# Kernel optimization log

Hardware: AMD Instinct MI355X
Metric: run time of the kernel (lower is better)

Reference implementation:

```python
import jax, jax.numpy as jnp
import numpy as np

N_HEAD = 16
D_K = 64
D_V = 64
D_MODEL = 1024
EPS = 1e-6
NEG = -1e9


def layer_norm(x, gamma, beta):
    mu = jnp.mean(x, axis=-1, keepdims=True)
    var = jnp.var(x, axis=-1, keepdims=True)
    return (x - mu) * jax.lax.rsqrt(var + EPS) * gamma + beta


def setup_inputs() -> dict:
    key = jax.random.key(0)
    ks = jax.random.split(key, 8)
    B, L = 2, 2048
    q = jax.random.normal(ks[0], (B, L, D_MODEL), dtype=jnp.float32)
    k = jax.random.normal(ks[1], (B, L, D_MODEL), dtype=jnp.float32)
    v = jax.random.normal(ks[2], (B, L, D_MODEL), dtype=jnp.float32)
    mask = jnp.ones((L, L), dtype=jnp.int32)
    s = 1.0 / np.sqrt(D_MODEL)
    w_q = jax.random.normal(ks[3], (N_HEAD * D_K, D_MODEL), dtype=jnp.float32) * s
    w_k = jax.random.normal(ks[4], (N_HEAD * D_K, D_MODEL), dtype=jnp.float32) * s
    w_v = jax.random.normal(ks[5], (N_HEAD * D_V, D_MODEL), dtype=jnp.float32) * s
    w_o = jax.random.normal(ks[6], (D_MODEL, N_HEAD * D_V), dtype=jnp.float32) * s
    ln_g = jnp.ones((D_MODEL,), dtype=jnp.float32)
    ln_b = jnp.zeros((D_MODEL,), dtype=jnp.float32)
    return {"q": q, "k": k, "v": v, "mask": mask,
            "w_q": w_q, "w_k": w_k, "w_v": w_v, "w_o": w_o,
            "ln_g": ln_g, "ln_b": ln_b}


def reference(q, k, v, mask, w_q, w_k, w_v, w_o, ln_g, ln_b):
    B, Lq, _ = q.shape
    Lk = k.shape[1]
    residual = q
    qn = layer_norm(q, ln_g, ln_b)
    # projections (nn.Linear: x @ W^T), reshape to [B, H, L, d]
    Q = (qn @ w_q.T).reshape(B, Lq, N_HEAD, D_K).transpose(0, 2, 1, 3)
    K = (k @ w_k.T).reshape(B, Lk, N_HEAD, D_K).transpose(0, 2, 1, 3)
    V = (v @ w_v.T).reshape(B, Lk, N_HEAD, D_V).transpose(0, 2, 1, 3)
    temp = jnp.asarray(D_K ** 0.5, dtype=Q.dtype)
    attn = jnp.einsum('bhqd,bhkd->bhqk', Q / temp, K)
    attn = jnp.where(mask[None, None] == 0, jnp.asarray(NEG, attn.dtype), attn)
    attn = jax.nn.softmax(attn, axis=-1)  # dropout is identity in eval
    out = jnp.einsum('bhqk,bhkd->bhqd', attn, V)
    out = out.transpose(0, 2, 1, 3).reshape(B, Lq, N_HEAD * D_V)
    out = out @ w_o.T
    return out + residual
```

## Files before the change

kernel.cpp:

```cpp
#include <hip/hip_runtime.h>
#include <stdint.h>

typedef __attribute__((ext_vector_type(8))) short bf16x8;
typedef __attribute__((ext_vector_type(4))) short s16x4;
typedef __attribute__((ext_vector_type(4))) float f32x4;

__device__ __forceinline__ ushort f2bf(float f) {
  union { float f; uint32_t u; } c; c.f = f;
  uint32_t r = (c.u + 0x7fffu + ((c.u >> 16) & 1u)) >> 16;
  return (ushort)r;
}

__device__ __forceinline__ void gload16(const void* g, void* l) {
  __builtin_amdgcn_global_load_lds(
      (const __attribute__((address_space(1))) void*)g,
      (__attribute__((address_space(3))) void*)l, 16, 0, 0);
}

__device__ __forceinline__ unsigned lds_addr(const void* p) {
  return (unsigned)(uintptr_t)(__attribute__((address_space(3))) const char*)p;
}

__device__ __forceinline__ uint32_t cvtpk(float lo, float hi) {
  uint32_t d;
  asm("v_cvt_pk_bf16_f32 %0, %1, %2" : "=v"(d) : "v"(lo), "v"(hi));
  return d;
}

__global__ __launch_bounds__(256) void prep_kernel(
    const float* __restrict__ q, const float* __restrict__ k,
    const float* __restrict__ v, const float* __restrict__ w_q,
    const float* __restrict__ w_k, const float* __restrict__ w_v,
    const float* __restrict__ w_o, const float* __restrict__ ln_g,
    const float* __restrict__ ln_b,
    ushort* __restrict__ qn, ushort* __restrict__ kb, ushort* __restrict__ vb,
    ushort* __restrict__ wqb, ushort* __restrict__ wkb,
    ushort* __restrict__ wvb, ushort* __restrict__ wob) {
  const int bid = blockIdx.x;
  const int t = threadIdx.x;
  if (bid < 4096) {
    const int row = bid;
    const float4 val = ((const float4*)(q + (size_t)row * 1024))[t];
    float s  = val.x + val.y + val.z + val.w;
    float s2 = val.x*val.x + val.y*val.y + val.z*val.z + val.w*val.w;
    #pragma unroll
    for (int off = 1; off < 64; off <<= 1) {
      s  += __shfl_xor(s,  off);
      s2 += __shfl_xor(s2, off);
    }
    __shared__ float red[8];
    const int wave = t >> 6, lane = t & 63;
    if (lane == 0) { red[wave*2] = s; red[wave*2+1] = s2; }
    __syncthreads();
    s  = red[0] + red[2] + red[4] + red[6];
    s2 = red[1] + red[3] + red[5] + red[7];
    const float mu = s * (1.0f/1024.0f);
    const float var = s2 * (1.0f/1024.0f) - mu*mu;
    const float rs = rsqrtf(var + 1e-6f);
    const float4 gg = ((const float4*)ln_g)[t];
    const float4 bb = ((const float4*)ln_b)[t];
    ushort4 o;
    o.x = f2bf((val.x - mu) * rs * gg.x + bb.x);
    o.y = f2bf((val.y - mu) * rs * gg.y + bb.y);
    o.z = f2bf((val.z - mu) * rs * gg.z + bb.z);
    o.w = f2bf((val.w - mu) * rs * gg.w + bb.w);
    ((ushort4*)(qn + (size_t)row * 1024))[t] = o;
    return;
  }
  const float* in; ushort* out; int i;
  if (bid < 12288) {
    const int idx = bid - 4096;
    const bool isv = idx >= 4096;
    in  = isv ? v : k;
    out = isv ? vb : kb;
    i = (idx & 4095) * 256 + t;
  } else {
    const int idx = bid - 12288;
    const int w = idx >> 10;
    in  = w == 0 ? w_q : (w == 1 ? w_k : (w == 2 ? w_v : w_o));
    out = w == 0 ? wqb : (w == 1 ? wkb : (w == 2 ? wvb : wob));
    i = (idx & 1023) * 256 + t;
  }
  const float4 val = ((const float4*)in)[i];
  ushort4 o;
  o.x = f2bf(val.x); o.y = f2bf(val.y); o.z = f2bf(val.z); o.w = f2bf(val.w);
  ((ushort4*)out)[i] = o;
}

__global__ __launch_bounds__(256) void mask_flags(
    const int* __restrict__ mask, int* __restrict__ flags) {
  const int qt = blockIdx.y, kt = blockIdx.x;
  const int t = threadIdx.x;
  const int* p = mask + (size_t)(qt * 64 + (t >> 2)) * 2048 + kt * 64 + (t & 3) * 16;
  int ok = 1;
  #pragma unroll
  for (int i = 0; i < 4; i++) {
    const int4 m = ((const int4*)p)[i];
    ok &= (m.x != 0) & (m.y != 0) & (m.z != 0) & (m.w != 0);
  }
  __shared__ int sok;
  if (t == 0) sok = 1;
  __syncthreads();
  if (!ok) atomicAnd(&sok, 0);
  __syncthreads();
  if (t == 0) flags[qt * 32 + kt] = sok;
}

__global__ __launch_bounds__(256, 3) void gemm3(
    const ushort* __restrict__ A0, const ushort* __restrict__ W0, ushort* __restrict__ C0,
    const ushort* __restrict__ A1, const ushort* __restrict__ W1, ushort* __restrict__ C1,
    const ushort* __restrict__ A2, const ushort* __restrict__ W2, ushort* __restrict__ C2,
    float qscale) {
  __shared__ ushort As[3][4096];
  __shared__ ushort Bs[3][4096];
  const int t = threadIdx.x, lane = t & 63, wave = t >> 6;
  const int wr = wave >> 1, wc = wave & 1;
  const int lr = lane & 15, lg = lane >> 4;
  const int lin = blockIdx.x;
  const int swz = (lin & 7) * 96 + (lin >> 3);
  const int brow = ((swz >> 3) & 31) * 128, bcol = (swz & 7) * 128;
  const int z = swz >> 8;
  const ushort* A = z == 0 ? A0 : (z == 1 ? A1 : A2);
  const ushort* W = z == 0 ? W0 : (z == 1 ? W1 : W2);
  ushort*      C = z == 0 ? C0 : (z == 1 ? C1 : C2);
  const float sc = (z == 0) ? qscale : 1.0f;
  f32x4 acc[4][4] = {};
  const int r_ = t >> 2, cx = (t & 3) ^ ((r_ >> 1) & 3);
  const ushort* gA  = A + (size_t)(brow + r_) * 1024 + cx * 8;
  const ushort* gB  = W + (size_t)(bcol + r_) * 1024 + cx * 8;
  const ushort* gA2 = gA + 64 * 1024;
  const ushort* gB2 = gB + 64 * 1024;
  const int woff = wave * 1024;
  char* const la0 = (char*)As[0] + woff;
  char* const la1 = (char*)As[1] + woff;
  char* const la2 = (char*)As[2] + woff;
  char* const lb0 = (char*)Bs[0] + woff;
  char* const lb1 = (char*)Bs[1] + woff;
  char* const lb2 = (char*)Bs[2] + woff;
  const int xA = ((lr >> 1) & 3) * 8;

#define G_ISSUE_U(LA, LB, OFF) { \
    gload16(gA  + (OFF), (LA));        gload16(gA2 + (OFF), (LA) + 4096); \
    gload16(gB  + (OFF), (LB));        gload16(gB2 + (OFF), (LB) + 4096); }

#define G_COMPUTE_U(BI) { \
    const ushort* as_ = As[BI]; \
    const ushort* bs_ = Bs[BI]; \
    bf16x8 af[4], bfr[4]; \
    _Pragma("unroll") for (int i = 0; i < 4; i++) \
      af[i]  = *(const bf16x8*)&as_[(wr*64 + i*16 + lr) * 32 + ((lg*8) ^ xA)]; \
    _Pragma("unroll") for (int i = 0; i < 4; i++) \
      bfr[i] = *(const bf16x8*)&bs_[(wc*64 + i*16 + lr) * 32 + ((lg*8) ^ xA)]; \
    _Pragma("unroll") for (int mi = 0; mi < 4; mi++) \
      _Pragma("unroll") for (int ni = 0; ni < 4; ni++) \
        acc[mi][ni] = __builtin_amdgcn_mfma_f32_16x16x32_bf16(af[mi], bfr[ni], acc[mi][ni], 0, 0, 0); }

  G_ISSUE_U(la0, lb0, 0);
  G_ISSUE_U(la1, lb1, 32);
  for (int k = 0; k < 10; ++k) {
    asm volatile("s_waitcnt vmcnt(4)" ::: "memory");
    __builtin_amdgcn_s_barrier();
    G_ISSUE_U(la2, lb2, 64);
    G_COMPUTE_U(0);
    asm volatile("s_waitcnt vmcnt(4)" ::: "memory");
    __builtin_amdgcn_s_barrier();
    G_ISSUE_U(la0, lb0, 96);
    G_COMPUTE_U(1);
    asm volatile("s_waitcnt vmcnt(4)" ::: "memory");
    __builtin_amdgcn_s_barrier();
    G_ISSUE_U(la1, lb1, 128);
    G_COMPUTE_U(2);
    gA += 96; gA2 += 96; gB += 96; gB2 += 96;
  }
  asm volatile("s_waitcnt vmcnt(4)" ::: "memory");
  __builtin_amdgcn_s_barrier();
  G_COMPUTE_U(0);
  asm volatile("s_waitcnt vmcnt(0)" ::: "memory");
  __builtin_amdgcn_s_barrier();
  G_COMPUTE_U(1);
#undef G_ISSUE_U
#undef G_COMPUTE_U

  #pragma unroll
  for (int mi = 0; mi < 4; mi++) {
    #pragma unroll
    for (int ni = 0; ni < 4; ni++) {
      #pragma unroll
      for (int r = 0; r < 4; r++) {
        const size_t row = brow + wr*64 + mi*16 + lg*4 + r;
        const size_t col = bcol + wc*64 + ni*16 + lr;
        C[row * 1024 + col] = f2bf(acc[mi][ni][r] * sc);
      }
    }
  }
}

__global__ __launch_bounds__(256) void gemm_bm64(
    const ushort* __restrict__ A, const ushort* __restrict__ W,
    float* __restrict__ Cf, const float* __restrict__ resid) {
  __shared__ ushort As[4][2048];
  __shared__ ushort Bs[4][4096];
  const int t = threadIdx.x, lane = t & 63, wave = t >> 6;
  const int wr = wave >> 1, wc = wave & 1;
  const int lr = lane & 15, lg = lane >> 4;
  const int lin = blockIdx.x;
  const int swz = (lin & 7) * 64 + (lin >> 3);
  const int brow = (swz >> 3) * 64, bcol = (swz & 7) * 128;
  f32x4 acc[2][4] = {};
  const int r_ = t >> 2, cx = (t & 3) ^ ((r_ >> 1) & 3);
  const ushort* gA = A + (size_t)(brow + r_) * 1024 + cx * 8;
  const ushort* gB = W + (size_t)(bcol + r_) * 1024 + cx * 8;
  const int woff = wave * 1024;
  const int xA = ((lr >> 1) & 3) * 8;

#define G_ISSUE(S) { \
    char* la = (char*)As + ((S) & 3) * 4096 + woff; \
    char* lb = (char*)Bs + ((S) & 3) * 8192 + woff; \
    const ushort* ap_ = gA + (S) * 32; \
    const ushort* bp_ = gB + (S) * 32; \
    gload16(ap_, la); \
    gload16(bp_, lb); gload16(bp_ + 64 * 1024, lb + 4096); }

#define G_COMPUTE(S) { \
    const ushort* as_ = As[(S) & 3]; \
    const ushort* bs_ = Bs[(S) & 3]; \
    bf16x8 af[2], bfr[4]; \
    _Pragma("unroll") for (int i = 0; i < 2; i++) \
      af[i]  = *(const bf16x8*)&as_[(wr*32 + i*16 + lr) * 32 + ((lg*8) ^ xA)]; \
    _Pragma("unroll") for (int i = 0; i < 4; i++) \
      bfr[i] = *(const bf16x8*)&bs_[(wc*64 + i*16 + lr) * 32 + ((lg*8) ^ xA)]; \
    _Pragma("unroll") for (int mi = 0; mi < 2; mi++) \
      _Pragma("unroll") for (int ni = 0; ni < 4; ni++) \
        acc[mi][ni] = __builtin_amdgcn_mfma_f32_16x16x32_bf16(af[mi], bfr[ni], acc[mi][ni], 0, 0, 0); }

  G_ISSUE(0); G_ISSUE(1); G_ISSUE(2);
  for (int s = 0; s < 30; ++s) {
    asm volatile("s_waitcnt vmcnt(6)" ::: "memory");
    __builtin_amdgcn_s_barrier();
    if (s < 29) G_ISSUE(s + 3);
    G_COMPUTE(s);
  }
  asm volatile("s_waitcnt vmcnt(3)" ::: "memory");
  __builtin_amdgcn_s_barrier();
  G_COMPUTE(30);
  asm volatile("s_waitcnt vmcnt(0)" ::: "memory");
  __builtin_amdgcn_s_barrier();
  G_COMPUTE(31);
#undef G_ISSUE
#undef G_COMPUTE

  #pragma unroll
  for (int mi = 0; mi < 2; mi++) {
    #pragma unroll
    for (int ni = 0; ni < 4; ni++) {
      #pragma unroll
      for (int r = 0; r < 4; r++) {
        const size_t row = brow + wr*32 + mi*16 + lg*4 + r;
        const size_t col = bcol + wc*64 + ni*16 + lr;
        Cf[row * 1024 + col] = acc[mi][ni][r] + resid[row * 1024 + col];
      }
    }
  }
}

__global__ __launch_bounds__(512) void flash_attn(
    const ushort* __restrict__ Qp, const ushort* __restrict__ Kp,
    const ushort* __restrict__ Vp, const int* __restrict__ mask,
    const int* __restrict__ tflags, ushort* __restrict__ AO) {
  const int L = 2048;
  const int lin = blockIdx.x;
  const int swzb = (lin & 7) * 32 + (lin >> 3);
  const int qb = swzb & 7, h = (swzb >> 3) & 15, b = swzb >> 7;
  const int t = threadIdx.x, lane = t & 63, wave = t >> 6;
  const int l15 = lane & 15, hg = lane >> 4;
  __shared__ ushort Ks[2][8192];
  __shared__ ushort Vs[2][8192];
  const size_t base = (size_t)b * L * 1024 + h * 64;
  const int qw0 = qb * 256 + wave * 32;

  bf16x8 qf[2][2];
  #pragma unroll
  for (int qt = 0; qt < 2; qt++)
    #pragma unroll
    for (int kc = 0; kc < 2; kc++)
      qf[qt][kc] = *(const bf16x8*)(Qp + base +
                     (size_t)(qw0 + qt*16 + l15) * 1024 + kc*32 + hg*8);

  f32x4 accO[2][4] = {};
  f32x4 accL[2] = {};
  const bf16x8 onef = {16256, 16256, 16256, 16256, 16256, 16256, 16256, 16256};

  const int r5 = t >> 3;
  const ushort* gK = Kp + base + (size_t)r5 * 1024 + ((t & 7) ^ (r5 & 7)) * 8;
  const int vkv = (t >> 5) * 4 + ((t & 7) >> 1);
  const int vd  = ((t >> 3) & 3) * 16 + (t & 1) * 8;
  const ushort* gV = Vp + base + (size_t)vkv * 1024 + vd;

  const unsigned vbase = lds_addr((const char*)Vs) + hg * 1024 + l15 * 8;

#define STAGE2(P, BUF) { \
    char* kb_ = (char*)Ks[BUF] + wave * 1024; \
    const ushort* gk_ = gK + (size_t)(2*(P)) * 65536; \
    gload16(gk_, kb_);           gload16(gk_ + 65536, kb_ + 8192); \
    char* vb_ = (char*)Vs[BUF] + wave * 1024; \
    const ushort* gv_ = gV + (size_t)(2*(P)) * 65536; \
    gload16(gv_, vb_);           gload16(gv_ + 65536, vb_ + 8192); }

#define TRREAD(VLO, VHI, VA, C) { \
    _Pragma("unroll") for (int dblk = 0; dblk < 4; dblk++) \
      asm volatile("ds_read_b64_tr_b16 %0, %2 offset:%3\n\t" \
                   "ds_read_b64_tr_b16 %1, %2 offset:%4" \
                   : "=v"(VLO[dblk]), "=v"(VHI[dblk]) \
                   : "v"(VA), "i"((C)*4096 + dblk*128), "i"((C)*4096 + dblk*128 + 512) \
                   : "memory"); }

  STAGE2(0, 0);
  const int flagBase = (qb * 4 + (wave >> 1)) * 32;

  for (int p = 0; p < 16; ++p) {
    asm volatile("s_waitcnt vmcnt(0)" ::: "memory");
    __builtin_amdgcn_s_barrier();
    if (p + 1 < 16) { STAGE2(p + 1, (p + 1) & 1); }

    #pragma unroll
    for (int half = 0; half < 2; ++half) {
      const int kvt = 2*p + half;
      const char* KsB = (const char*)Ks[p & 1] + half * 8192;
      const unsigned va = vbase + (p & 1) * 16384 + half * 8192;

      f32x4 s[2][4] = {};
      const int rx16 = (l15 & 7) << 4;
      __builtin_amdgcn_s_setprio(1);
      #pragma unroll
      for (int kc = 0; kc < 2; kc++) {
        const int cb = (kc*64 + hg*16) ^ rx16;
        const bf16x8 k0 = *(const bf16x8*)(KsB + (     l15) * 128 + cb);
        const bf16x8 k1 = *(const bf16x8*)(KsB + (16 + l15) * 128 + cb);
        const bf16x8 k2 = *(const bf16x8*)(KsB + (32 + l15) * 128 + cb);
        const bf16x8 k3 = *(const bf16x8*)(KsB + (48 + l15) * 128 + cb);
        #pragma unroll
        for (int qt = 0; qt < 2; qt++) {
          s[qt][0] = __builtin_amdgcn_mfma_f32_16x16x32_bf16(k0, qf[qt][kc], s[qt][0], 0, 0, 0);
          s[qt][1] = __builtin_amdgcn_mfma_f32_16x16x32_bf16(k1, qf[qt][kc], s[qt][1], 0, 0, 0);
          s[qt][2] = __builtin_amdgcn_mfma_f32_16x16x32_bf16(k2, qf[qt][kc], s[qt][2], 0, 0, 0);
          s[qt][3] = __builtin_amdgcn_mfma_f32_16x16x32_bf16(k3, qf[qt][kc], s[qt][3], 0, 0, 0);
        }
      }
      __builtin_amdgcn_s_setprio(0);

      s16x4 vlo[4], vhi[4];
      TRREAD(vlo, vhi, va, 0);

      if (tflags[flagBase + kvt] == 0) {
        #pragma unroll
        for (int qt = 0; qt < 2; qt++) {
          const size_t mrow = (size_t)(qw0 + qt*16 + l15) * L + kvt * 64;
          #pragma unroll
          for (int r = 0; r < 4; ++r) {
            const int kvr = hg*4 + r;
            if (mask[mrow + kvr] == 0)      s[qt][0][r] = -1e9f;
            if (mask[mrow + 16 + kvr] == 0) s[qt][1][r] = -1e9f;
            if (mask[mrow + 32 + kvr] == 0) s[qt][2][r] = -1e9f;
            if (mask[mrow + 48 + kvr] == 0) s[qt][3][r] = -1e9f;
          }
        }
      }

      #pragma unroll
      for (int qt = 0; qt < 2; qt++)
        #pragma unroll
        for (int ni = 0; ni < 4; ++ni)
          #pragma unroll
          for (int r = 0; r < 4; ++r)
            s[qt][ni][r] = __builtin_amdgcn_exp2f(s[qt][ni][r]);

      union U8 { uint32_t u[4]; bf16x8 v; };
      bf16x8 pa[2][2];
      #pragma unroll
      for (int qt = 0; qt < 2; qt++) {
        #pragma unroll
        for (int c = 0; c < 2; ++c) {
          const f32x4& ta = s[qt][2*c];
          const f32x4& tb = s[qt][2*c + 1];
          uint32_t A = cvtpk(ta[0], ta[1]), B = cvtpk(ta[2], ta[3]);
          uint32_t C = cvtpk(tb[0], tb[1]), D = cvtpk(tb[2], tb[3]);
          asm("v_permlane32_swap_b32 %0, %1" : "+v"(A), "+v"(C));
          asm("v_permlane16_swap_b32 %0, %1" : "+v"(A), "+v"(C));
          asm("v_permlane32_swap_b32 %0, %1" : "+v"(B), "+v"(D));
          asm("v_permlane16_swap_b32 %0, %1" : "+v"(B), "+v"(D));
          U8 f; f.u[0] = A; f.u[1] = B; f.u[2] = C; f.u[3] = D;
          pa[qt][c] = f.v;
        }
      }

      asm volatile("s_waitcnt lgkmcnt(0)" ::: "memory");
      __builtin_amdgcn_sched_barrier(0);
      __builtin_amdgcn_s_setprio(1);
      #pragma unroll
      for (int dblk = 0; dblk < 4; dblk++) {
        const bf16x8 bv = __builtin_shufflevector(vlo[dblk], vhi[dblk],
                                                  0, 1, 2, 3, 4, 5, 6, 7);
        accO[0][dblk] = __builtin_amdgcn_mfma_f32_16x16x32_bf16(pa[0][0], bv, accO[0][dblk], 0, 0, 0);
        accO[1][dblk] = __builtin_amdgcn_mfma_f32_16x16x32_bf16(pa[1][0], bv, accO[1][dblk], 0, 0, 0);
      }
      accL[0] = __builtin_amdgcn_mfma_f32_16x16x32_bf16(pa[0][0], onef, accL[0], 0, 0, 0);
      accL[1] = __builtin_amdgcn_mfma_f32_16x16x32_bf16(pa[1][0], onef, accL[1], 0, 0, 0);
      __builtin_amdgcn_s_setprio(0);

      TRREAD(vlo, vhi, va, 1);
      asm volatile("s_waitcnt lgkmcnt(0)" ::: "memory");
      __builtin_amdgcn_sched_barrier(0);
      __builtin_amdgcn_s_setprio(1);
      #pragma unroll
      for (int dblk = 0; dblk < 4; dblk++) {
        const bf16x8 bv = __builtin_shufflevector(vlo[dblk], vhi[dblk],
                                                  0, 1, 2, 3, 4, 5, 6, 7);
        accO[0][dblk] = __builtin_amdgcn_mfma_f32_16x16x32_bf16(pa[0][1], bv, accO[0][dblk], 0, 0, 0);
        accO[1][dblk] = __builtin_amdgcn_mfma_f32_16x16x32_bf16(pa[1][1], bv, accO[1][dblk], 0, 0, 0);
      }
      accL[0] = __builtin_amdgcn_mfma_f32_16x16x32_bf16(pa[0][1], onef, accL[0], 0, 0, 0);
      accL[1] = __builtin_amdgcn_mfma_f32_16x16x32_bf16(pa[1][1], onef, accL[1], 0, 0, 0);
      __builtin_amdgcn_s_setprio(0);
    }
  }

  #pragma unroll
  for (int qt = 0; qt < 2; qt++) {
    #pragma unroll
    for (int r = 0; r < 4; ++r) {
      const float inv = 1.0f / accL[qt][r];
      const size_t row = (size_t)b * L + qw0 + qt*16 + hg*4 + r;
      #pragma unroll
      for (int dblk = 0; dblk < 4; dblk++)
        AO[row * 1024 + h*64 + dblk*16 + l15] = f2bf(accO[qt][dblk][r] * inv);
    }
  }
#undef STAGE2
#undef TRREAD
}

extern "C" void kernel_launch(void* const* d_in, const int* in_sizes, int n_in,
                              void* d_out, int out_size, void* d_ws, size_t ws_size,
                              hipStream_t stream) {
  const float* q    = (const float*)d_in[0];
  const float* k    = (const float*)d_in[1];
  const float* v    = (const float*)d_in[2];
  const int*   mask = (const int*)d_in[3];
  const float* w_q  = (const float*)d_in[4];
  const float* w_k  = (const float*)d_in[5];
  const float* w_v  = (const float*)d_in[6];
  const float* w_o  = (const float*)d_in[7];
  const float* ln_g = (const float*)d_in[8];
  const float* ln_b = (const float*)d_in[9];
  float* out = (float*)d_out;

  char* ws = (char*)d_ws;
  const size_t MB = (size_t)1 << 20;
  ushort* qn  = (ushort*)(ws + 0*MB);
  ushort* kb  = (ushort*)(ws + 8*MB);
  ushort* vb  = (ushort*)(ws + 16*MB);
  ushort* wqb = (ushort*)(ws + 24*MB);
  ushort* wkb = (ushort*)(ws + 26*MB);
  ushort* wvb = (ushort*)(ws + 28*MB);
  ushort* wob = (ushort*)(ws + 30*MB);
  ushort* Qp  = (ushort*)(ws + 32*MB);
  ushort* Kp  = (ushort*)(ws + 40*MB);
  ushort* Vp  = (ushort*)(ws + 48*MB);
  ushort* AO  = (ushort*)(ws + 56*MB);
  int* tflags = (int*)(ws + 8*MB);

  const float QSCALE = 0.125f * 1.44269504089f;

  prep_kernel<<<16384, 256, 0, stream>>>(
      q, k, v, w_q, w_k, w_v, w_o, ln_g, ln_b,
      qn, kb, vb, wqb, wkb, wvb, wob);

  gemm3<<<768, 256, 0, stream>>>(
      qn, wqb, Qp, kb, wkb, Kp, vb, wvb, Vp, QSCALE);

  mask_flags<<<dim3(32, 32), 256, 0, stream>>>(mask, tflags);

  flash_attn<<<256, 512, 0, stream>>>(Qp, Kp, Vp, mask, tflags, AO);

  gemm_bm64<<<512, 256, 0, stream>>>(AO, wob, out, q);
}
```

Measured before the change: 121.8 us.

## Split attention KV range across two blocks and combine partial results

The flash attention kernel now splits each (batch, head, q-block) work item into two halves of the KV sequence, launching 512 blocks instead of 256. Each block writes unnormalized partial outputs in bf16 plus row sums, and a new combine kernel adds the two halves and normalizes into AO. This is meant to raise occupancy and fill the GPU's compute units better, since 256 blocks underfill the device. The cost is an extra kernel launch, extra global traffic for the partials, halved LDS staging per iteration, and an extra bf16 rounding of the partial sums. Because there is no running max, summing the two halves stays valid.

```diff
diff --git a/kernel.cpp b/kernel.cpp
--- a/kernel.cpp
+++ b/kernel.cpp
@@ -9,6 +9,10 @@
   union { float f; uint32_t u; } c; c.f = f;
   uint32_t r = (c.u + 0x7fffu + ((c.u >> 16) & 1u)) >> 16;
   return (ushort)r;
+}
+
+__device__ __forceinline__ float bf2f(ushort u) {
+  return __uint_as_float((uint32_t)u << 16);
 }
 
 __device__ __forceinline__ void gload16(const void* g, void* l) {
@@ -266,17 +270,21 @@
 __global__ __launch_bounds__(512) void flash_attn(
     const ushort* __restrict__ Qp, const ushort* __restrict__ Kp,
     const ushort* __restrict__ Vp, const int* __restrict__ mask,
-    const int* __restrict__ tflags, ushort* __restrict__ AO) {
+    const int* __restrict__ tflags,
+    ushort* __restrict__ P0, ushort* __restrict__ P1,
+    float* __restrict__ l0, float* __restrict__ l1) {
   const int L = 2048;
   const int lin = blockIdx.x;
-  const int swzb = (lin & 7) * 32 + (lin >> 3);
-  const int qb = swzb & 7, h = (swzb >> 3) & 15, b = swzb >> 7;
+  const int swzb = (lin & 7) * 64 + (lin >> 3);
+  const int split = swzb & 1, qb = (swzb >> 1) & 7;
+  const int h = (swzb >> 4) & 15, b = swzb >> 8;
   const int t = threadIdx.x, lane = t & 63, wave = t >> 6;
   const int l15 = lane & 15, hg = lane >> 4;
-  __shared__ ushort Ks[2][8192];
-  __shared__ ushort Vs[2][8192];
+  __shared__ ushort Ks[2][4096];
+  __shared__ ushort Vs[2][4096];
   const size_t base = (size_t)b * L * 1024 + h * 64;
   const int qw0 = qb * 256 + wave * 32;
+  const int T0 = split * 16;
 
   bf16x8 qf[2][2];
   #pragma unroll
@@ -298,13 +306,9 @@
 
   const unsigned vbase = lds_addr((const char*)Vs) + hg * 1024 + l15 * 8;
 
-#define STAGE2(P, BUF) { \
-    char* kb_ = (char*)Ks[BUF] + wave * 1024; \
-    const ushort* gk_ = gK + (size_t)(2*(P)) * 65536; \
-    gload16(gk_, kb_);           gload16(gk_ + 65536, kb_ + 8192); \
-    char* vb_ = (char*)Vs[BUF] + wave * 1024; \
-    const ushort* gv_ = gV + (size_t)(2*(P)) * 65536; \
-    gload16(gv_, vb_);           gload16(gv_ + 65536, vb_ + 8192); }
+#define STAGE(T, BUF) { \
+    gload16(gK + (size_t)(T) * 65536, (char*)Ks[BUF] + wave * 1024); \
+    gload16(gV + (size_t)(T) * 65536, (char*)Vs[BUF] + wave * 1024); }
 
 #define TRREAD(VLO, VHI, VA, C) { \
     _Pragma("unroll") for (int dblk = 0; dblk < 4; dblk++) \
@@ -314,129 +318,147 @@
                    : "v"(VA), "i"((C)*4096 + dblk*128), "i"((C)*4096 + dblk*128 + 512) \
                    : "memory"); }
 
-  STAGE2(0, 0);
+  STAGE(T0, 0);
   const int flagBase = (qb * 4 + (wave >> 1)) * 32;
 
-  for (int p = 0; p < 16; ++p) {
+  for (int s = 0; s < 16; ++s) {
     asm volatile("s_waitcnt vmcnt(0)" ::: "memory");
     __builtin_amdgcn_s_barrier();
-    if (p + 1 < 16) { STAGE2(p + 1, (p + 1) & 1); }
-
-    #pragma unroll
-    for (int half = 0; half < 2; ++half) {
-      const int kvt = 2*p + half;
-      const char* KsB = (const char*)Ks[p & 1] + half * 8192;
-      const unsigned va = vbase + (p & 1) * 16384 + half * 8192;
-
-      f32x4 s[2][4] = {};
-      const int rx16 = (l15 & 7) << 4;
-      __builtin_amdgcn_s_setprio(1);
-      #pragma unroll
-      for (int kc = 0; kc < 2; kc++) {
-        const int cb = (kc*64 + hg*16) ^ rx16;
-        const bf16x8 k0 = *(const bf16x8*)(KsB + (     l15) * 128 + cb);
-        const bf16x8 k1 = *(const bf16x8*)(KsB + (16 + l15) * 128 + cb);
-        const bf16x8 k2 = *(const bf16x8*)(KsB + (32 + l15) * 128 + cb);
-        const bf16x8 k3 = *(const bf16x8*)(KsB + (48 + l15) * 128 + cb);
+    if (s + 1 < 16) { STAGE(T0 + s + 1, (s + 1) & 1); }
+
+    const int kvt = T0 + s;
+    const char* KsB = (const char*)Ks[s & 1];
+    const unsigned va = vbase + (s & 1) * 8192;
+
+    f32x4 sc[2][4] = {};
+    const int rx16 = (l15 & 7) << 4;
+    __builtin_amdgcn_s_setprio(1);
+    #pragma unroll
+    for (int kc = 0; kc < 2; kc++) {
+      const int cb = (kc*64 + hg*16) ^ rx16;
+      const bf16x8 k0 = *(const bf16x8*)(KsB + (     l15) * 128 + cb);
+      const bf16x8 k1 = *(const bf16x8*)(KsB + (16 + l15) * 128 + cb);
+      const bf16x8 k2 = *(const bf16x8*)(KsB + (32 + l15) * 128 + cb);
+      const bf16x8 k3 = *(const bf16x8*)(KsB + (48 + l15) * 128 + cb);
+      #pragma unroll
+      for (int qt = 0; qt < 2; qt++) {
+        sc[qt][0] = __builtin_amdgcn_mfma_f32_16x16x32_bf16(k0, qf[qt][kc], sc[qt][0], 0, 0, 0);
+        sc[qt][1] = __builtin_amdgcn_mfma_f32_16x16x32_bf16(k1, qf[qt][kc], sc[qt][1], 0, 0, 0);
+        sc[qt][2] = __builtin_amdgcn_mfma_f32_16x16x32_bf16(k2, qf[qt][kc], sc[qt][2], 0, 0, 0);
+        sc[qt][3] = __builtin_amdgcn_mfma_f32_16x16x32_bf16(k3, qf[qt][kc], sc[qt][3], 0, 0, 0);
+      }
+    }
+    __builtin_amdgcn_s_setprio(0);
+
+    s16x4 vlo[4], vhi[4];
+    TRREAD(vlo, vhi, va, 0);
+
+    if (tflags[flagBase + kvt] == 0) {
+      #pragma unroll
+      for (int qt = 0; qt < 2; qt++) {
+        const size_t mrow = (size_t)(qw0 + qt*16 + l15) * L + kvt * 64;
         #pragma unroll
-        for (int qt = 0; qt < 2; qt++) {
-          s[qt][0] = __builtin_amdgcn_mfma_f32_16x16x32_bf16(k0, qf[qt][kc], s[qt][0], 0, 0, 0);
-          s[qt][1] = __builtin_amdgcn_mfma_f32_16x16x32_bf16(k1, qf[qt][kc], s[qt][1], 0, 0, 0);
-          s[qt][2] = __builtin_amdgcn_mfma_f32_16x16x32_bf16(k2, qf[qt][kc], s[qt][2], 0, 0, 0);
-          s[qt][3] = __builtin_amdgcn_mfma_f32_16x16x32_bf16(k3, qf[qt][kc], s[qt][3], 0, 0, 0);
+        for (int r = 0; r < 4; ++r) {
+          const int kvr = hg*4 + r;
+          if (mask[mrow + kvr] == 0)      sc[qt][0][r] = -1e9f;
+          if (mask[mrow + 16 + kvr] == 0) sc[qt][1][r] = -1e9f;
+          if (mask[mrow + 32 + kvr] == 0) sc[qt][2][r] = -1e9f;
+          if (mask[mrow + 48 + kvr] == 0) sc[qt][3][r] = -1e9f;
         }
       }
-      __builtin_amdgcn_s_setprio(0);
-
-      s16x4 vlo[4], vhi[4];
-      TRREAD(vlo, vhi, va, 0);
-
-      if (tflags[flagBase + kvt] == 0) {
+    }
+
+    #pragma unroll
+    for (int qt = 0; qt < 2; qt++)
+      #pragma unroll
+      for (int ni = 0; ni < 4; ++ni)
         #pragma unroll
-        for (int qt = 0; qt < 2; qt++) {
-          const size_t mrow = (size_t)(qw0 + qt*16 + l15) * L + kvt * 64;
-          #pragma unroll
-          for (int r = 0; r < 4; ++r) {
-            const int kvr = hg*4 + r;
-            if (mask[mrow + kvr] == 0)      s[qt][0][r] = -1e9f;
-            if (mask[mrow + 16 + kvr] == 0) s[qt][1][r] = -1e9f;
-            if (mask[mrow + 32 + kvr] == 0) s[qt][2][r] = -1e9f;
-            if (mask[mrow + 48 + kvr] == 0) s[qt][3][r] = -1e9f;
-          }
-        }
+        for (int r = 0; r < 4; ++r)
+          sc[qt][ni][r] = __builtin_amdgcn_exp2f(sc[qt][ni][r]);
+
+    union U8 { uint32_t u[4]; bf16x8 v; };
+    bf16x8 pa[2][2];
+    #pragma unroll
+    for (int qt = 0; qt < 2; qt++) {
+      #pragma unroll
+      for (int c = 0; c < 2; ++c) {
+        const f32x4& ta = sc[qt][2*c];
+        const f32x4& tb = sc[qt][2*c + 1];
+        uint32_t A = cvtpk(ta[0], ta[1]), B = cvtpk(ta[2], ta[3]);
+        uint32_t C = cvtpk(tb[0], tb[1]), D = cvtpk(tb[2], tb[3]);
+        asm("v_permlane32_swap_b32 %0, %1" : "+v"(A), "+v"(C));
+        asm("v_permlane16_swap_b32 %0, %1" : "+v"(A), "+v"(C));
+        asm("v_permlane32_swap_b32 %0, %1" : "+v"(B), "+v"(D));
+        asm("v_permlane16_swap_b32 %0, %1" : "+v"(B), "+v"(D));
+        U8 f; f.u[0] = A; f.u[1] = B; f.u[2] = C; f.u[3] = D;
+        pa[qt][c] = f.v;
       }
-
-      #pragma unroll
-      for (int qt = 0; qt < 2; qt++)
-        #pragma unroll
-        for (int ni = 0; ni < 4; ++ni)
-          #pragma unroll
-          for (int r = 0; r < 4; ++r)
-            s[qt][ni][r] = __builtin_amdgcn_exp2f(s[qt][ni][r]);
-
-      union U8 { uint32_t u[4]; bf16x8 v; };
-      bf16x8 pa[2][2];
-      #pragma unroll
-      for (int qt = 0; qt < 2; qt++) {
-        #pragma unroll
-        for (int c = 0; c < 2; ++c) {
-          const f32x4& ta = s[qt][2*c];
-          const f32x4& tb = s[qt][2*c + 1];
-          uint32_t A = cvtpk(ta[0], ta[1]), B = cvtpk(ta[2], ta[3]);
-          uint32_t C = cvtpk(tb[0], tb[1]), D = cvtpk(tb[2], tb[3]);
-          asm("v_permlane32_swap_b32 %0, %1" : "+v"(A), "+v"(C));
-          asm("v_permlane16_swap_b32 %0, %1" : "+v"(A), "+v"(C));
-          asm("v_permlane32_swap_b32 %0, %1" : "+v"(B), "+v"(D));
-          asm("v_permlane16_swap_b32 %0, %1" : "+v"(B), "+v"(D));
-          U8 f; f.u[0] = A; f.u[1] = B; f.u[2] = C; f.u[3] = D;
-          pa[qt][c] = f.v;
-        }
-      }
-
-      asm volatile("s_waitcnt lgkmcnt(0)" ::: "memory");
-      __builtin_amdgcn_sched_barrier(0);
-      __builtin_amdgcn_s_setprio(1);
-      #pragma unroll
-      for (int dblk = 0; dblk < 4; dblk++) {
-        const bf16x8 bv = __builtin_shufflevector(vlo[dblk], vhi[dblk],
-                                                  0, 1, 2, 3, 4, 5, 6, 7);
-        accO[0][dblk] = __builtin_amdgcn_mfma_f32_16x16x32_bf16(pa[0][0], bv, accO[0][dblk], 0, 0, 0);
-        accO[1][dblk] = __builtin_amdgcn_mfma_f32_16x16x32_bf16(pa[1][0], bv, accO[1][dblk], 0, 0, 0);
-      }
-      accL[0] = __builtin_amdgcn_mfma_f32_16x16x32_bf16(pa[0][0], onef, accL[0], 0, 0, 0);
-      accL[1] = __builtin_amdgcn_mfma_f32_16x16x32_bf16(pa[1][0], onef, accL[1], 0, 0, 0);
-      __builtin_amdgcn_s_setprio(0);
-
-      TRREAD(vlo, vhi, va, 1);
-      asm volatile("s_waitcnt lgkmcnt(0)" ::: "memory");
-      __builtin_amdgcn_sched_barrier(0);
-      __builtin_amdgcn_s_setprio(1);
-      #pragma unroll
-      for (int dblk = 0; dblk < 4; dblk++) {
-        const bf16x8 bv = __builtin_shufflevector(vlo[dblk], vhi[dblk],
-                                                  0, 1, 2, 3, 4, 5, 6, 7);
-        accO[0][dblk] = __builtin_amdgcn_mfma_f32_16x16x32_bf16(pa[0][1], bv, accO[0][dblk], 0, 0, 0);
-        accO[1][dblk] = __builtin_amdgcn_mfma_f32_16x16x32_bf16(pa[1][1], bv, accO[1][dblk], 0, 0, 0);
-      }
-      accL[0] = __builtin_amdgcn_mfma_f32_16x16x32_bf16(pa[0][1], onef, accL[0], 0, 0, 0);
-      accL[1] = __builtin_amdgcn_mfma_f32_16x16x32_bf16(pa[1][1], onef, accL[1], 0, 0, 0);
-      __builtin_amdgcn_s_setprio(0);
-    }
-  }
-
+    }
+
+    asm volatile("s_waitcnt lgkmcnt(0)" ::: "memory");
+    __builtin_amdgcn_sched_barrier(0);
+    __builtin_amdgcn_s_setprio(1);
+    #pragma unroll
+    for (int dblk = 0; dblk < 4; dblk++) {
+      const bf16x8 bv = __builtin_shufflevector(vlo[dblk], vhi[dblk],
+                                                0, 1, 2, 3, 4, 5, 6, 7);
+      accO[0][dblk] = __builtin_amdgcn_mfma_f32_16x16x32_bf16(pa[0][0], bv, accO[0][dblk], 0, 0, 0);
+      accO[1][dblk] = __builtin_amdgcn_mfma_f32_16x16x32_bf16(pa[1][0], bv, accO[1][dblk], 0, 0, 0);
+    }
+    accL[0] = __builtin_amdgcn_mfma_f32_16x16x32_bf16(pa[0][0], onef, accL[0], 0, 0, 0);
+    accL[1] = __builtin_amdgcn_mfma_f32_16x16x32_bf16(pa[1][0], onef, accL[1], 0, 0, 0);
+    __builtin_amdgcn_s_setprio(0);
+
+    TRREAD(vlo, vhi, va, 1);
+    asm volatile("s_waitcnt lgkmcnt(0)" ::: "memory");
+    __builtin_amdgcn_sched_barrier(0);
+    __builtin_amdgcn_s_setprio(1);
+    #pragma unroll
+    for (int dblk = 0; dblk < 4; dblk++) {
+      const bf16x8 bv = __builtin_shufflevector(vlo[dblk], vhi[dblk],
+                                                0, 1, 2, 3, 4, 5, 6, 7);
+      accO[0][dblk] = __builtin_amdgcn_mfma_f32_16x16x32_bf16(pa[0][1], bv, accO[0][dblk], 0, 0, 0);
+      accO[1][dblk] = __builtin_amdgcn_mfma_f32_16x16x32_bf16(pa[1][1], bv, accO[1][dblk], 0, 0, 0);
+    }
+    accL[0] = __builtin_amdgcn_mfma_f32_16x16x32_bf16(pa[0][1], onef, accL[0], 0, 0, 0);
+    accL[1] = __builtin_amdgcn_mfma_f32_16x16x32_bf16(pa[1][1], onef, accL[1], 0, 0, 0);
+    __builtin_amdgcn_s_setprio(0);
+  }
+
+  ushort* Pout = split ? P1 : P0;
+  float*  lout = split ? l1 : l0;
   #pragma unroll
   for (int qt = 0; qt < 2; qt++) {
     #pragma unroll
     for (int r = 0; r < 4; ++r) {
-      const float inv = 1.0f / accL[qt][r];
       const size_t row = (size_t)b * L + qw0 + qt*16 + hg*4 + r;
       #pragma unroll
       for (int dblk = 0; dblk < 4; dblk++)
-        AO[row * 1024 + h*64 + dblk*16 + l15] = f2bf(accO[qt][dblk][r] * inv);
-    }
-  }
-#undef STAGE2
+        Pout[row * 1024 + h*64 + dblk*16 + l15] = f2bf(accO[qt][dblk][r]);
+      if (l15 == 0) lout[row * 16 + h] = accL[qt][r];
+    }
+  }
+#undef STAGE
 #undef TRREAD
+}
+
+__global__ __launch_bounds__(256) void combine_kernel(
+    const ushort* __restrict__ P0, const ushort* __restrict__ P1,
+    const float* __restrict__ l0, const float* __restrict__ l1,
+    ushort* __restrict__ AO) {
+  const int i = blockIdx.x * 256 + threadIdx.x;
+  const int row = i >> 7;
+  const int h = (i >> 3) & 15;
+  const float inv = 1.0f / (l0[row * 16 + h] + l1[row * 16 + h]);
+  const uint4 A = ((const uint4*)P0)[i];
+  const uint4 C = ((const uint4*)P1)[i];
+  const ushort* ua = (const ushort*)&A;
+  const ushort* uc = (const ushort*)&C;
+  union { ushort us[8]; uint4 v; } o;
+  #pragma unroll
+  for (int j = 0; j < 8; j++)
+    o.us[j] = f2bf((bf2f(ua[j]) + bf2f(uc[j])) * inv);
+  ((uint4*)AO)[i] = o.v;
 }
 
 extern "C" void kernel_launch(void* const* d_in, const int* in_sizes, int n_in,
@@ -467,7 +489,11 @@
   ushort* Kp  = (ushort*)(ws + 40*MB);
   ushort* Vp  = (ushort*)(ws + 48*MB);
   ushort* AO  = (ushort*)(ws + 56*MB);
-  int* tflags = (int*)(ws + 8*MB);
+  ushort* P0  = (ushort*)(ws + 0*MB);
+  ushort* P1  = (ushort*)(ws + 8*MB);
+  float*  l0  = (float*)(ws + 16*MB);
+  float*  l1  = (float*)(ws + 16*MB + 256*1024);
+  int* tflags = (int*)(ws + 16*MB + 512*1024);
 
   const float QSCALE = 0.125f * 1.44269504089f;
 
@@ -480,7 +506,10 @@
 
   mask_flags<<<dim3(32, 32), 256, 0, stream>>>(mask, tflags);
 
-  flash_attn<<<256, 512, 0, stream>>>(Qp, Kp, Vp, mask, tflags, AO);
+  flash_attn<<<512, 512, 0, stream>>>(
+      Qp, Kp, Vp, mask, tflags, P0, P1, l0, l1);
+
+  combine_kernel<<<2048, 256, 0, stream>>>(P0, P1, l0, l1, AO);
 
   gemm_bm64<<<512, 256, 0, stream>>>(AO, wob, out, q);
 }
```

Result: slower. 136.5 us (+12.1%).
